# Performance work log

Hardware: AMD Instinct MI355X
Metric: run time of the kernel (lower is better)

Reference implementation:

```python
import jax, jax.numpy as jnp
import numpy as np

C_IN = 5
KERNEL = 4
DEPTH = 4
C = C_IN + 3  # original + time + 2 CNN channels


def conv1d(x, w, b):
    # x: (B, Cin, L), w: (Cout, Cin, K) -> (B, Cout, L-K+1), 'VALID' padding as in signatory.Augment defaults
    y = jax.lax.conv_general_dilated(x, w, (1,), 'VALID',
                                     dimension_numbers=('NCH', 'OIH', 'NCH'))
    return y + b[None, :, None]


def augment(inp, w1, b1, w2, b2, w3, b3):
    # inp: (B, L, C_in). Mirrors signatory.Augment with layer_sizes=(8,8,2), kernel_size=4,
    # include_original=True, include_time=True, activation=relu (between layers, not after last).
    B, L, _ = inp.shape
    trunc = KERNEL - 1
    orig = inp[:, trunc:, :]                                   # (B, L-3, C_in)
    time = jnp.linspace(0.0, 1.0, L, dtype=inp.dtype)[trunc:]  # time over original stream, truncated
    time = jnp.broadcast_to(time[None, :, None], (B, L - trunc, 1))
    h = conv1d(inp.transpose(0, 2, 1), w1, b1)   # (B, 8, L-3)
    h = conv1d(jax.nn.relu(h), w2, b2)           # (B, 8, L-3)
    h = conv1d(jax.nn.relu(h), w3, b3)           # (B, 2, L-3)
    return jnp.concatenate([orig, time, h.transpose(0, 2, 1)], axis=2)  # (B, L-3, C)


def signature(path):
    # Truncated path signature, depth 4, basepoint=True (zero basepoint prepended).
    # Chen's relation: sig <- sig (tensor) exp(dx), maintained as per-level tensors.
    B, S, Cc = path.shape
    base = jnp.zeros((B, 1, Cc), path.dtype)
    inc = jnp.diff(jnp.concatenate([base, path], axis=1), axis=1)  # (B, S, C) increments incl. basepoint
    inc = inc.transpose(1, 0, 2)  # (S, B, C) for scan

    def step(carry, dx):
        s1, s2, s3, s4 = carry
        # exp(dx) levels: dx^(k)/k!
        e1 = dx
        e2 = jnp.einsum('bi,bj->bij', dx, dx) / 2.0
        e3 = jnp.einsum('bij,bk->bijk', e2, dx) / 3.0
        e4 = jnp.einsum('bijk,bl->bijkl', e3, dx) / 4.0
        # Chen: (A (x) B)_k = sum_i A_i (x) B_{k-i}, A_0 = B_0 = 1
        n1 = s1 + e1
        n2 = s2 + e2 + jnp.einsum('bi,bj->bij', s1, e1)
        n3 = (s3 + e3 + jnp.einsum('bi,bjk->bijk', s1, e2)
              + jnp.einsum('bij,bk->bijk', s2, e1))
        n4 = (s4 + e4 + jnp.einsum('bi,bjkl->bijkl', s1, e3)
              + jnp.einsum('bij,bkl->bijkl', s2, e2)
              + jnp.einsum('bijk,bl->bijkl', s3, e1))
        return (n1, n2, n3, n4), None

    init = (jnp.zeros((B, Cc), path.dtype),
            jnp.zeros((B, Cc, Cc), path.dtype),
            jnp.zeros((B, Cc, Cc, Cc), path.dtype),
            jnp.zeros((B, Cc, Cc, Cc, Cc), path.dtype))
    (s1, s2, s3, s4), _ = jax.lax.scan(step, init, inc)
    return jnp.concatenate([s1.reshape(B, -1), s2.reshape(B, -1),
                            s3.reshape(B, -1), s4.reshape(B, -1)], axis=1)  # (B, 4680)


def setup_inputs() -> dict:
    key = jax.random.key(0)
    ks = jax.random.split(key, 4)
    B, L = 64, 256

    def init_conv(k, cout, cin, ksz):
        bound = 1.0 / np.sqrt(cin * ksz)
        kw, kb = jax.random.split(k)
        w = jax.random.uniform(kw, (cout, cin, ksz), jnp.float32, -bound, bound)
        b = jax.random.uniform(kb, (cout,), jnp.float32, -bound, bound)
        return w, b

    w1, b1 = init_conv(ks[1], 8, C_IN, KERNEL)
    w2, b2 = init_conv(ks[2], 8, 8, 1)
    w3, b3 = init_conv(ks[3], 2, 8, 1)
    inp = jax.random.normal(ks[0], (B, L, C_IN), jnp.float32)
    return {"inp": inp, "w1": w1, "b1": b1, "w2": w2, "b2": b2, "w3": w3, "b3": b3}


def reference(inp, w1, b1, w2, b2, w3, b3):
    x = augment(inp, w1, b1, w2, b2, w3, b3)  # (B, L-3, C)
    return signature(x)                       # (B, 4680)
```

## Files before the change

### kernel.cpp

```cpp
#include <hip/hip_runtime.h>

#define L_IN    256
#define S_STEPS 253
#define CIN     5

template<int I>
__device__ __forceinline__ void scan_and_store(
    const float (* __restrict__ dxs)[8], int j, int k, int b, int lane,
    float* __restrict__ out)
{
    float s1 = 0.f, s2 = 0.f, s3 = 0.f;
    float s4[8];
    #pragma unroll
    for (int l = 0; l < 8; ++l) s4[l] = 0.f;

    const float4* __restrict__ dx4 = reinterpret_cast<const float4*>(&dxs[0][0]);

    float own_p[4], bb_p[4];
    float4 r0_p[4], r1_p[4];
    #pragma unroll
    for (int u = 0; u < 4; ++u) {
        own_p[u] = dxs[u][k];
        bb_p[u]  = dxs[u][j];
        r0_p[u]  = dx4[2 * u];
        r1_p[u]  = dx4[2 * u + 1];
    }

    for (int tb = 0; tb < 256; tb += 4) {
        #pragma unroll
        for (int u = 0; u < 4; ++u) {
            const int tn = tb + u + 4;
            float  own_n = dxs[tn][k];
            float  bb_n  = dxs[tn][j];
            float4 r0_n  = dx4[2 * tn];
            float4 r1_n  = dx4[2 * tn + 1];

            const float own = own_p[u];
            const float bb  = bb_p[u];
            const float4 r0 = r0_p[u];
            const float4 r1 = r1_p[u];
            const float a =
                (I == 0) ? r0.x : (I == 1) ? r0.y : (I == 2) ? r0.z :
                (I == 3) ? r0.w : (I == 4) ? r1.x : (I == 5) ? r1.y :
                (I == 6) ? r1.z : r1.w;

            const float t2    = fmaf(a, 0.5f, s1);
            const float t3    = fmaf(s1, 0.5f, a * (1.0f / 6.0f));
            const float t4    = fmaf(s1, (1.0f / 6.0f), a * (1.0f / 24.0f));
            const float coef3 = fmaf(bb, t3, s2);
            const float uu    = fmaf(bb, t4, 0.5f * s2);
            const float coef4 = fmaf(own, uu, s3);
            s4[0] = fmaf(coef4, r0.x, s4[0]);
            s4[1] = fmaf(coef4, r0.y, s4[1]);
            s4[2] = fmaf(coef4, r0.z, s4[2]);
            s4[3] = fmaf(coef4, r0.w, s4[3]);
            s4[4] = fmaf(coef4, r1.x, s4[4]);
            s4[5] = fmaf(coef4, r1.y, s4[5]);
            s4[6] = fmaf(coef4, r1.z, s4[6]);
            s4[7] = fmaf(coef4, r1.w, s4[7]);
            s3 = fmaf(coef3, own, s3);
            s2 = fmaf(t2, bb, s2);
            s1 += a;

            own_p[u] = own_n; bb_p[u] = bb_n;
            r0_p[u] = r0_n;   r1_p[u] = r1_n;
        }
    }

    float* __restrict__ ob = out + (size_t)b * 4680;
    if (lane == 0) ob[I] = s1;
    if (k == 0)    ob[8 + I * 8 + j] = s2;
    ob[72 + (I * 8 + j) * 8 + k] = s3;
    float4* o4 = reinterpret_cast<float4*>(ob + 584 + (size_t)((I * 8 + j) * 8 + k) * 8);
    o4[0] = make_float4(s4[0], s4[1], s4[2], s4[3]);
    o4[1] = make_float4(s4[4], s4[5], s4[6], s4[7]);
}

__global__ __launch_bounds__(64) void fused_sig_kernel(
    const float* __restrict__ inp,
    const float* __restrict__ w1, const float* __restrict__ b1,
    const float* __restrict__ w2, const float* __restrict__ b2,
    const float* __restrict__ w3, const float* __restrict__ b3,
    float* __restrict__ out)
{
    const int blk = blockIdx.x;
    const int b   = blk >> 3;
    const int i   = blk & 7;
    const int tid = threadIdx.x;

    __shared__ float path[S_STEPS][8];
    __shared__ __align__(16) float dxs[264][8];

    const float* __restrict__ x = inp + b * (L_IN * CIN);
    #pragma unroll
    for (int p = 0; p < 4; ++p) {
        const int t = tid + p * 64;
        if (t < S_STEPS) {
            float h1[8];
            #pragma unroll
            for (int o = 0; o < 8; ++o) h1[o] = b1[o];
            #pragma unroll
            for (int kk = 0; kk < 4; ++kk) {
                #pragma unroll
                for (int ci = 0; ci < CIN; ++ci) {
                    float v = x[(t + kk) * CIN + ci];
                    #pragma unroll
                    for (int o = 0; o < 8; ++o) h1[o] = fmaf(v, w1[o * 20 + ci * 4 + kk], h1[o]);
                }
            }
            float r1v[8];
            #pragma unroll
            for (int o = 0; o < 8; ++o) r1v[o] = h1[o] > 0.f ? h1[o] : 0.f;
            float h2[8];
            #pragma unroll
            for (int o = 0; o < 8; ++o) h2[o] = b2[o];
            #pragma unroll
            for (int q = 0; q < 8; ++q) {
                #pragma unroll
                for (int o = 0; o < 8; ++o) h2[o] = fmaf(r1v[q], w2[o * 8 + q], h2[o]);
            }
            float r2v[8];
            #pragma unroll
            for (int o = 0; o < 8; ++o) r2v[o] = h2[o] > 0.f ? h2[o] : 0.f;
            float h30 = b3[0], h31 = b3[1];
            #pragma unroll
            for (int q = 0; q < 8; ++q) {
                h30 = fmaf(r2v[q], w3[q], h30);
                h31 = fmaf(r2v[q], w3[8 + q], h31);
            }
            #pragma unroll
            for (int c = 0; c < 5; ++c) path[t][c] = x[(t + 3) * CIN + c];
            path[t][5] = (float)(t + 3) * (1.0f / 255.0f);
            path[t][6] = h30;
            path[t][7] = h31;
        }
    }
    dxs[253 + (tid >> 3)][tid & 7] = 0.f;
    __syncthreads();
    #pragma unroll
    for (int p = 0; p < 4; ++p) {
        const int t = tid + p * 64;
        if (t < S_STEPS) {
            #pragma unroll
            for (int c = 0; c < 8; ++c) {
                float prev = (t > 0) ? path[t - 1][c] : 0.f;
                dxs[t][c] = path[t][c] - prev;
            }
        }
    }
    __syncthreads();

    const int lane = tid;
    const int j    = lane >> 3;
    const int k    = lane & 7;
    switch (i) {
        case 0: scan_and_store<0>(dxs, j, k, b, lane, out); break;
        case 1: scan_and_store<1>(dxs, j, k, b, lane, out); break;
        case 2: scan_and_store<2>(dxs, j, k, b, lane, out); break;
        case 3: scan_and_store<3>(dxs, j, k, b, lane, out); break;
        case 4: scan_and_store<4>(dxs, j, k, b, lane, out); break;
        case 5: scan_and_store<5>(dxs, j, k, b, lane, out); break;
        case 6: scan_and_store<6>(dxs, j, k, b, lane, out); break;
        default: scan_and_store<7>(dxs, j, k, b, lane, out); break;
    }
}

extern "C" void kernel_launch(void* const* d_in, const int* in_sizes, int n_in,
                              void* d_out, int out_size, void* d_ws, size_t ws_size,
                              hipStream_t stream)
{
    const float* inp = (const float*)d_in[0];
    const float* w1  = (const float*)d_in[1];
    const float* b1  = (const float*)d_in[2];
    const float* w2  = (const float*)d_in[3];
    const float* b2  = (const float*)d_in[4];
    const float* w3  = (const float*)d_in[5];
    const float* b3  = (const float*)d_in[6];
    float* out = (float*)d_out;

    fused_sig_kernel<<<512, 64, 0, stream>>>(inp, w1, b1, w2, b2, w3, b3, out);
}
```

Baseline: 85.34 us.

## Split signature scan into time chunks and combine with Chen's identity

Replaces the single sequential 256-step scan per (batch, row) block with 8 time chunks of 32 steps each. Every block now computes the partial signature of one chunk across 8 waves and writes it to a workspace. A second kernel folds the 8 chunk signatures per batch with Chen's product. This cuts the serial dependency chain length and raises parallelism, at the cost of a second launch, workspace traffic and extra combine arithmetic.

```diff
diff --git a/kernel.cpp b/kernel.cpp
--- a/kernel.cpp
+++ b/kernel.cpp
@@ -3,11 +3,59 @@
 #define L_IN    256
 #define S_STEPS 253
 #define CIN     5
+#define CH_LEN  32
+#define SIG_N   4680
+
+__device__ __forceinline__ void path_row(
+    const float* __restrict__ x, int r,
+    const float* __restrict__ w1, const float* __restrict__ b1,
+    const float* __restrict__ w2, const float* __restrict__ b2,
+    const float* __restrict__ w3, const float* __restrict__ b3,
+    float o[8])
+{
+    float h1[8];
+    #pragma unroll
+    for (int q = 0; q < 8; ++q) h1[q] = b1[q];
+    #pragma unroll
+    for (int kk = 0; kk < 4; ++kk) {
+        #pragma unroll
+        for (int ci = 0; ci < CIN; ++ci) {
+            float v = x[(r + kk) * CIN + ci];
+            #pragma unroll
+            for (int q = 0; q < 8; ++q) h1[q] = fmaf(v, w1[q * 20 + ci * 4 + kk], h1[q]);
+        }
+    }
+    float r1v[8];
+    #pragma unroll
+    for (int q = 0; q < 8; ++q) r1v[q] = h1[q] > 0.f ? h1[q] : 0.f;
+    float h2[8];
+    #pragma unroll
+    for (int q = 0; q < 8; ++q) h2[q] = b2[q];
+    #pragma unroll
+    for (int p = 0; p < 8; ++p) {
+        #pragma unroll
+        for (int q = 0; q < 8; ++q) h2[q] = fmaf(r1v[p], w2[q * 8 + p], h2[q]);
+    }
+    float r2v[8];
+    #pragma unroll
+    for (int q = 0; q < 8; ++q) r2v[q] = h2[q] > 0.f ? h2[q] : 0.f;
+    float h30 = b3[0], h31 = b3[1];
+    #pragma unroll
+    for (int p = 0; p < 8; ++p) {
+        h30 = fmaf(r2v[p], w3[p], h30);
+        h31 = fmaf(r2v[p], w3[8 + p], h31);
+    }
+    #pragma unroll
+    for (int cc = 0; cc < 5; ++cc) o[cc] = x[(r + 3) * CIN + cc];
+    o[5] = (float)(r + 3) * (1.0f / 255.0f);
+    o[6] = h30;
+    o[7] = h31;
+}
 
 template<int I>
-__device__ __forceinline__ void scan_and_store(
-    const float (* __restrict__ dxs)[8], int j, int k, int b, int lane,
-    float* __restrict__ out)
+__device__ __forceinline__ void chunk_scan(
+    const float (* __restrict__ dxs)[8], int j, int k, int lane,
+    float* __restrict__ wsig)
 {
     float s1 = 0.f, s2 = 0.f, s3 = 0.f;
     float s4[8];
@@ -26,7 +74,7 @@
         r1_p[u]  = dx4[2 * u + 1];
     }
 
-    for (int tb = 0; tb < 256; tb += 4) {
+    for (int tb = 0; tb < CH_LEN; tb += 4) {
         #pragma unroll
         for (int u = 0; u < 4; ++u) {
             const int tn = tb + u + 4;
@@ -67,102 +115,148 @@
         }
     }
 
-    float* __restrict__ ob = out + (size_t)b * 4680;
-    if (lane == 0) ob[I] = s1;
-    if (k == 0)    ob[8 + I * 8 + j] = s2;
-    ob[72 + (I * 8 + j) * 8 + k] = s3;
-    float4* o4 = reinterpret_cast<float4*>(ob + 584 + (size_t)((I * 8 + j) * 8 + k) * 8);
+    if (lane == 0) wsig[I] = s1;
+    if (k == 0)    wsig[8 + I * 8 + j] = s2;
+    wsig[72 + (I * 8 + j) * 8 + k] = s3;
+    float4* o4 = reinterpret_cast<float4*>(wsig + 584 + (size_t)((I * 8 + j) * 8 + k) * 8);
     o4[0] = make_float4(s4[0], s4[1], s4[2], s4[3]);
     o4[1] = make_float4(s4[4], s4[5], s4[6], s4[7]);
 }
 
-__global__ __launch_bounds__(64) void fused_sig_kernel(
+__global__ __launch_bounds__(512) void chunk_sig_kernel(
     const float* __restrict__ inp,
     const float* __restrict__ w1, const float* __restrict__ b1,
     const float* __restrict__ w2, const float* __restrict__ b2,
     const float* __restrict__ w3, const float* __restrict__ b3,
-    float* __restrict__ out)
+    float* __restrict__ ws)
 {
     const int blk = blockIdx.x;
     const int b   = blk >> 3;
-    const int i   = blk & 7;
+    const int c   = blk & 7;
     const int tid = threadIdx.x;
 
-    __shared__ float path[S_STEPS][8];
-    __shared__ __align__(16) float dxs[264][8];
+    __shared__ __align__(16) float pbuf[33][8];
+    __shared__ __align__(16) float dxs[36][8];
 
     const float* __restrict__ x = inp + b * (L_IN * CIN);
-    #pragma unroll
-    for (int p = 0; p < 4; ++p) {
-        const int t = tid + p * 64;
-        if (t < S_STEPS) {
-            float h1[8];
-            #pragma unroll
-            for (int o = 0; o < 8; ++o) h1[o] = b1[o];
-            #pragma unroll
-            for (int kk = 0; kk < 4; ++kk) {
-                #pragma unroll
-                for (int ci = 0; ci < CIN; ++ci) {
-                    float v = x[(t + kk) * CIN + ci];
-                    #pragma unroll
-                    for (int o = 0; o < 8; ++o) h1[o] = fmaf(v, w1[o * 20 + ci * 4 + kk], h1[o]);
-                }
-            }
-            float r1v[8];
-            #pragma unroll
-            for (int o = 0; o < 8; ++o) r1v[o] = h1[o] > 0.f ? h1[o] : 0.f;
-            float h2[8];
-            #pragma unroll
-            for (int o = 0; o < 8; ++o) h2[o] = b2[o];
-            #pragma unroll
-            for (int q = 0; q < 8; ++q) {
-                #pragma unroll
-                for (int o = 0; o < 8; ++o) h2[o] = fmaf(r1v[q], w2[o * 8 + q], h2[o]);
-            }
-            float r2v[8];
-            #pragma unroll
-            for (int o = 0; o < 8; ++o) r2v[o] = h2[o] > 0.f ? h2[o] : 0.f;
-            float h30 = b3[0], h31 = b3[1];
-            #pragma unroll
-            for (int q = 0; q < 8; ++q) {
-                h30 = fmaf(r2v[q], w3[q], h30);
-                h31 = fmaf(r2v[q], w3[8 + q], h31);
-            }
-            #pragma unroll
-            for (int c = 0; c < 5; ++c) path[t][c] = x[(t + 3) * CIN + c];
-            path[t][5] = (float)(t + 3) * (1.0f / 255.0f);
-            path[t][6] = h30;
-            path[t][7] = h31;
-        }
-    }
-    dxs[253 + (tid >> 3)][tid & 7] = 0.f;
+
+    if (tid < 33) {
+        const int r = CH_LEN * c - 1 + tid;
+        if (r >= 0 && r <= 252) {
+            float o[8];
+            path_row(x, r, w1, b1, w2, b2, w3, b3, o);
+            #pragma unroll
+            for (int ch = 0; ch < 8; ++ch) pbuf[tid][ch] = o[ch];
+        } else {
+            #pragma unroll
+            for (int ch = 0; ch < 8; ++ch) pbuf[tid][ch] = 0.f;
+        }
+    }
+    if (tid >= 64 && tid < 96) {
+        dxs[32 + ((tid - 64) >> 3)][tid & 7] = 0.f;
+    }
     __syncthreads();
-    #pragma unroll
-    for (int p = 0; p < 4; ++p) {
-        const int t = tid + p * 64;
-        if (t < S_STEPS) {
-            #pragma unroll
-            for (int c = 0; c < 8; ++c) {
-                float prev = (t > 0) ? path[t - 1][c] : 0.f;
-                dxs[t][c] = path[t][c] - prev;
-            }
+    if (tid < CH_LEN) {
+        const int tg = CH_LEN * c + tid;
+        if (tg <= 252) {
+            #pragma unroll
+            for (int ch = 0; ch < 8; ++ch)
+                dxs[tid][ch] = pbuf[tid + 1][ch] - pbuf[tid][ch];
+        } else {
+            #pragma unroll
+            for (int ch = 0; ch < 8; ++ch) dxs[tid][ch] = 0.f;
         }
     }
     __syncthreads();
 
-    const int lane = tid;
+    const int wave = tid >> 6;
+    const int lane = tid & 63;
     const int j    = lane >> 3;
     const int k    = lane & 7;
-    switch (i) {
-        case 0: scan_and_store<0>(dxs, j, k, b, lane, out); break;
-        case 1: scan_and_store<1>(dxs, j, k, b, lane, out); break;
-        case 2: scan_and_store<2>(dxs, j, k, b, lane, out); break;
-        case 3: scan_and_store<3>(dxs, j, k, b, lane, out); break;
-        case 4: scan_and_store<4>(dxs, j, k, b, lane, out); break;
-        case 5: scan_and_store<5>(dxs, j, k, b, lane, out); break;
-        case 6: scan_and_store<6>(dxs, j, k, b, lane, out); break;
-        default: scan_and_store<7>(dxs, j, k, b, lane, out); break;
-    }
+    float* __restrict__ wsig = ws + (size_t)(b * 8 + c) * SIG_N;
+    switch (wave) {
+        case 0: chunk_scan<0>(dxs, j, k, lane, wsig); break;
+        case 1: chunk_scan<1>(dxs, j, k, lane, wsig); break;
+        case 2: chunk_scan<2>(dxs, j, k, lane, wsig); break;
+        case 3: chunk_scan<3>(dxs, j, k, lane, wsig); break;
+        case 4: chunk_scan<4>(dxs, j, k, lane, wsig); break;
+        case 5: chunk_scan<5>(dxs, j, k, lane, wsig); break;
+        case 6: chunk_scan<6>(dxs, j, k, lane, wsig); break;
+        default: chunk_scan<7>(dxs, j, k, lane, wsig); break;
+    }
+}
+
+__global__ __launch_bounds__(512) void fold_kernel(
+    const float* __restrict__ ws, float* __restrict__ out)
+{
+    const int b    = blockIdx.x;
+    const int tid  = threadIdx.x;
+    const int i    = tid >> 6;
+    const int lane = tid & 63;
+    const int j    = lane >> 3;
+    const int k    = lane & 7;
+    const int row  = ((i * 8 + j) * 8 + k) * 8;
+
+    __shared__ __align__(16) float lsig[8 * 592];
+
+    float4 g0[8], g1[8];
+    #pragma unroll
+    for (int c = 0; c < 8; ++c) {
+        const float* p4 = ws + (size_t)(b * 8 + c) * SIG_N + 584 + row;
+        g0[c] = *reinterpret_cast<const float4*>(p4);
+        g1[c] = *reinterpret_cast<const float4*>(p4 + 4);
+    }
+    #pragma unroll
+    for (int c = 0; c < 8; ++c) {
+        const float* sb = ws + (size_t)(b * 8 + c) * SIG_N;
+        lsig[c * 592 + tid] = sb[tid];
+        if (tid < 72) lsig[c * 592 + 512 + tid] = sb[512 + tid];
+    }
+    __syncthreads();
+
+    float s1A = lsig[i];
+    float s2A = lsig[8 + i * 8 + j];
+    float s3A = lsig[72 + (i * 8 + j) * 8 + k];
+    float s4A[8] = { g0[0].x, g0[0].y, g0[0].z, g0[0].w,
+                     g1[0].x, g1[0].y, g1[0].z, g1[0].w };
+
+    #pragma unroll
+    for (int c = 1; c < 8; ++c) {
+        const float* __restrict__ lp = lsig + c * 592;
+        const float4 s1r0 = *reinterpret_cast<const float4*>(lp);
+        const float4 s1r1 = *reinterpret_cast<const float4*>(lp + 4);
+        const float4 s2r0 = *reinterpret_cast<const float4*>(lp + 8 + k * 8);
+        const float4 s2r1 = *reinterpret_cast<const float4*>(lp + 8 + k * 8 + 4);
+        const float4 s3r0 = *reinterpret_cast<const float4*>(lp + 72 + (j * 8 + k) * 8);
+        const float4 s3r1 = *reinterpret_cast<const float4*>(lp + 72 + (j * 8 + k) * 8 + 4);
+        const float s3B_ijk = lp[72 + (i * 8 + j) * 8 + k];
+        const float s2B_jk  = lp[8 + j * 8 + k];
+        const float s2B_ij  = lp[8 + i * 8 + j];
+        const float s1B_i   = lp[i];
+        const float s1B_j   = lp[j];
+        const float s1B_k   = lp[k];
+
+        s4A[0] = fmaf(s1A, s3r0.x, fmaf(s2A, s2r0.x, fmaf(s3A, s1r0.x, s4A[0] + g0[c].x)));
+        s4A[1] = fmaf(s1A, s3r0.y, fmaf(s2A, s2r0.y, fmaf(s3A, s1r0.y, s4A[1] + g0[c].y)));
+        s4A[2] = fmaf(s1A, s3r0.z, fmaf(s2A, s2r0.z, fmaf(s3A, s1r0.z, s4A[2] + g0[c].z)));
+        s4A[3] = fmaf(s1A, s3r0.w, fmaf(s2A, s2r0.w, fmaf(s3A, s1r0.w, s4A[3] + g0[c].w)));
+        s4A[4] = fmaf(s1A, s3r1.x, fmaf(s2A, s2r1.x, fmaf(s3A, s1r1.x, s4A[4] + g1[c].x)));
+        s4A[5] = fmaf(s1A, s3r1.y, fmaf(s2A, s2r1.y, fmaf(s3A, s1r1.y, s4A[5] + g1[c].y)));
+        s4A[6] = fmaf(s1A, s3r1.z, fmaf(s2A, s2r1.z, fmaf(s3A, s1r1.z, s4A[6] + g1[c].z)));
+        s4A[7] = fmaf(s1A, s3r1.w, fmaf(s2A, s2r1.w, fmaf(s3A, s1r1.w, s4A[7] + g1[c].w)));
+        const float s3n = fmaf(s1A, s2B_jk, fmaf(s2A, s1B_k, s3A + s3B_ijk));
+        const float s2n = fmaf(s1A, s1B_j, s2A + s2B_ij);
+        const float s1n = s1A + s1B_i;
+        s3A = s3n; s2A = s2n; s1A = s1n;
+    }
+
+    float* __restrict__ ob = out + (size_t)b * SIG_N;
+    if (lane == 0) ob[i] = s1A;
+    if (k == 0)    ob[8 + i * 8 + j] = s2A;
+    ob[72 + (i * 8 + j) * 8 + k] = s3A;
+    float4* o4 = reinterpret_cast<float4*>(ob + 584 + (size_t)row);
+    o4[0] = make_float4(s4A[0], s4A[1], s4A[2], s4A[3]);
+    o4[1] = make_float4(s4A[4], s4A[5], s4A[6], s4A[7]);
 }
 
 extern "C" void kernel_launch(void* const* d_in, const int* in_sizes, int n_in,
@@ -177,6 +271,8 @@
     const float* w3  = (const float*)d_in[5];
     const float* b3  = (const float*)d_in[6];
     float* out = (float*)d_out;
-
-    fused_sig_kernel<<<512, 64, 0, stream>>>(inp, w1, b1, w2, b2, w3, b3, out);
-}
+    float* ws  = (float*)d_ws;
+
+    chunk_sig_kernel<<<512, 512, 0, stream>>>(inp, w1, b1, w2, b2, w3, b3, ws);
+    fold_kernel<<<64, 512, 0, stream>>>(ws, out);
+}
```

New measurement: 134.5 us. 1.58x slower.
